# Kernel optimization log

Hardware: AMD Instinct MI355X
Metric: run time of the kernel (lower is better)

The kernel has to match this reference:

```python
import jax, jax.numpy as jnp
import numpy as np

KH, KW = 3, 3
STRIDE, PAD, DIL = 1, 1, 1


def setup_inputs() -> dict:
    key = jax.random.key(0)
    k1, k2, k3 = jax.random.split(key, 3)
    B, C, H, W, O = 8, 128, 64, 64, 128
    x = jax.random.normal(k1, (B, C, H, W), jnp.float32)
    # offset layout: [B, 2*K, Ho, Wo], pairs (dy, dx) per kernel tap
    offset = jax.random.normal(k2, (B, 2 * KH * KW, H, W), jnp.float32)
    n = C * KH * KW
    stdv = 1.0 / np.sqrt(n)
    weight = jax.random.uniform(k3, (O, C, KH, KW), jnp.float32, -stdv, stdv)
    bias = jnp.zeros((O,), jnp.float32)
    return {"x": x, "offset": offset, "weight": weight, "bias": bias}


def _deform_conv(x, offset, weight, bias):
    B, C, H, W = x.shape
    O = weight.shape[0]
    K = KH * KW
    Ho = (H + 2 * PAD - DIL * (KH - 1) - 1) // STRIDE + 1
    Wo = (W + 2 * PAD - DIL * (KW - 1) - 1) // STRIDE + 1

    off = offset.reshape(B, K, 2, Ho, Wo)  # (dy, dx) per tap

    # base sampling grid for each kernel tap: [K, Ho, Wo]
    hs = jnp.arange(Ho, dtype=jnp.float32) * STRIDE - PAD
    ws = jnp.arange(Wo, dtype=jnp.float32) * STRIDE - PAD
    ki = jnp.arange(KH, dtype=jnp.float32) * DIL
    kj = jnp.arange(KW, dtype=jnp.float32) * DIL
    base_y = (ki[:, None, None, None] + hs[None, None, :, None])  # [KH,1,Ho,1]
    base_x = (kj[None, :, None, None] + ws[None, None, None, :])  # [1,KW,1,Wo]
    base_y = jnp.broadcast_to(base_y, (KH, KW, Ho, Wo)).reshape(K, Ho, Wo)
    base_x = jnp.broadcast_to(base_x, (KH, KW, Ho, Wo)).reshape(K, Ho, Wo)

    py = base_y[None] + off[:, :, 0]  # [B,K,Ho,Wo]
    px = base_x[None] + off[:, :, 1]

    y0 = jnp.floor(py)
    x0 = jnp.floor(px)
    ly = py - y0  # fractional parts
    lx = px - x0
    y0i = y0.astype(jnp.int32)
    x0i = x0.astype(jnp.int32)

    flat = x.reshape(B, C, H * W)

    def gather(yi, xi, w):
        # zero outside the image (DCN zero-padding semantics)
        valid = (yi >= 0) & (yi < H) & (xi >= 0) & (xi < W)
        idx = jnp.clip(yi, 0, H - 1) * W + jnp.clip(xi, 0, W - 1)  # [B,K,Ho,Wo]
        g = jnp.take_along_axis(flat, idx.reshape(B, 1, -1), axis=2)
        g = g.reshape(B, C, K, Ho, Wo)
        wmask = (w * valid.astype(x.dtype))[:, None]  # [B,1,K,Ho,Wo]
        return g * wmask

    # bilinear accumulation over 4 corners -> im2col columns [B,C,K,Ho,Wo]
    cols = gather(y0i, x0i, (1 - ly) * (1 - lx))
    cols = cols + gather(y0i, x0i + 1, (1 - ly) * lx)
    cols = cols + gather(y0i + 1, x0i, ly * (1 - lx))
    cols = cols + gather(y0i + 1, x0i + 1, ly * lx)

    out = jnp.einsum('ock,bckhw->bohw', weight.reshape(O, C, K), cols)
    return out + bias[None, :, None, None]


def reference(x, offset, weight, bias):
    return _deform_conv(x, offset, weight, bias)
```

## Files before the change

kernel.cpp:

```cpp
#include <hip/hip_runtime.h>


#define BB 8
#define CC 128
#define HH 64
#define WW 64
#define OO 128
#define KTAPS 9

typedef __attribute__((ext_vector_type(8))) short bf16x8;
typedef __attribute__((ext_vector_type(4))) float f32x4;

__device__ __forceinline__ unsigned short f2bf(float f) {
    unsigned u = __float_as_uint(f);
    u += 0x7FFFu + ((u >> 16) & 1u);
    return (unsigned short)(u >> 16);
}
#if __has_builtin(__builtin_amdgcn_cvt_pk_bf16_f32)
typedef __attribute__((ext_vector_type(2))) __bf16 bf16x2_t;
__device__ __forceinline__ unsigned pack2bf(float lo, float hi) {
    bf16x2_t v = __builtin_amdgcn_cvt_pk_bf16_f32(lo, hi);
    unsigned r;
    __builtin_memcpy(&r, &v, 4);
    return r;
}
#else
__device__ __forceinline__ unsigned pack2bf(float lo, float hi) {
    return (unsigned)f2bf(lo) | ((unsigned)f2bf(hi) << 16);
}
#endif
__device__ __forceinline__ float bflo(unsigned p) { return __uint_as_float(p << 16); }
__device__ __forceinline__ float bfhi(unsigned p) { return __uint_as_float(p & 0xFFFF0000u); }

__global__ __launch_bounds__(256)
void prep_kernel(const float* __restrict__ x, const float* __restrict__ wgt,
                 unsigned short* __restrict__ xt, unsigned short* __restrict__ wpk) {
    const int t = threadIdx.x;
    if (blockIdx.x < 512) {
        __shared__ float tile[WW * 132];
        const int b = blockIdx.x >> 6;
        const int h = blockIdx.x & 63;
        const float* src = x + ((size_t)b * CC * HH + h) * WW;
        {
            const int wq = t & 15;
            const int cb = t >> 4;
#pragma unroll
            for (int it = 0; it < 8; ++it) {
                const int c = it * 16 + cb;
                const float4 v = *reinterpret_cast<const float4*>(src + (size_t)c * (HH * WW) + wq * 4);
                tile[(wq * 4 + 0) * 132 + c] = v.x;
                tile[(wq * 4 + 1) * 132 + c] = v.y;
                tile[(wq * 4 + 2) * 132 + c] = v.z;
                tile[(wq * 4 + 3) * 132 + c] = v.w;
            }
        }
        __syncthreads();
        unsigned short* dst = xt + ((size_t)b * HH + h) * WW * CC;
        {
            const int cg = t & 15;
            const int wb = t >> 4;
#pragma unroll
            for (int it = 0; it < 4; ++it) {
                const int w = it * 16 + wb;
                const float* tp = &tile[w * 132 + cg * 8];
                uint4 p;
                p.x = pack2bf(tp[0], tp[1]);
                p.y = pack2bf(tp[2], tp[3]);
                p.z = pack2bf(tp[4], tp[5]);
                p.w = pack2bf(tp[6], tp[7]);
                *reinterpret_cast<uint4*>(&dst[(size_t)w * CC + cg * 8]) = p;
            }
        }
    } else {
        const int id   = (blockIdx.x - 512) * 256 + t;
        const int lane = id & 63;
        const int frag = id >> 6;
        const int nt   = frag & 7;
        const int c0q  = (frag >> 3) & 3;
        const int tap  = frag >> 5;
        const int o    = (nt << 4) + (lane & 15);
        const int c    = (c0q << 5) + ((lane >> 4) << 3);
        const float* s = wgt + ((size_t)o * CC + c) * KTAPS + tap;
        unsigned u[4];
#pragma unroll
        for (int j = 0; j < 4; ++j)
            u[j] = pack2bf(s[(2 * j) * KTAPS], s[(2 * j + 1) * KTAPS]);
        *reinterpret_cast<uint4*>(wpk + (size_t)frag * 512 + lane * 8) =
            make_uint4(u[0], u[1], u[2], u[3]);
    }
}

__global__ __launch_bounds__(256, 2)
void dcn_mfma_kernel(const unsigned short* __restrict__ xt,
                     const unsigned short* __restrict__ wpk,
                     const float* __restrict__ offset,
                     const float* __restrict__ bias,
                     float* __restrict__ out) {
    __shared__ __align__(16) float smem_f[4 * 128 * 20];
    float2* sLL = reinterpret_cast<float2*>(smem_f);
    short2* sYX = reinterpret_cast<short2*>(smem_f + 1152);

    const int t  = threadIdx.x;
    const int b  = blockIdx.x >> 6;
    const int ho = blockIdx.x & 63;

    for (int s = t; s < KTAPS * 64; s += 256) {
        const int k  = s >> 6;
        const int wo = s & 63;
        const int ki = k / 3;
        const int kj = k - ki * 3;
        const float dy = offset[(((size_t)b * 18 + 2 * k    ) * 64 + ho) * 64 + wo];
        const float dx = offset[(((size_t)b * 18 + 2 * k + 1) * 64 + ho) * 64 + wo];
        const float py = (float)(ho - 1 + ki) + dy;
        const float px = (float)(wo - 1 + kj) + dx;
        const float y0f = floorf(py);
        const float x0f = floorf(px);
        sLL[s] = make_float2(py - y0f, px - x0f);
        sYX[s] = make_short2((short)(int)y0f, (short)(int)x0f);
    }
    __syncthreads();

    f32x4 acc[8];
#pragma unroll
    for (int nt = 0; nt < 8; ++nt) acc[nt] = (f32x4){0.f, 0.f, 0.f, 0.f};

    const int lane = t & 63;
    const int wave = t >> 6;
    const int lm   = lane & 15;
    const int quad = lane >> 4;
    const int q16  = quad * 16;
    const int lane16 = lane * 16;
    const char* xb = (const char*)(xt + (size_t)b * HH * WW * CC);
    const char* wb = (const char*)wpk;

    for (int tap = 0; tap < KTAPS; ++tap) {
        const int rec = (tap << 6) + (wave << 4) + lm;
        const float2 ll = sLL[rec];
        const short2 yx = sYX[rec];
        const int y0 = yx.x, x0 = yx.y;
        const int y1 = y0 + 1, x1 = x0 + 1;
        const float ly = ll.x, lx = ll.y;
        const bool vy0 = ((unsigned)y0 < (unsigned)HH);
        const bool vy1 = ((unsigned)y1 < (unsigned)HH);
        const bool vx0 = ((unsigned)x0 < (unsigned)WW);
        const bool vx1 = ((unsigned)x1 < (unsigned)WW);
        const float w00 = (vy0 && vx0) ? (1.f - ly) * (1.f - lx) : 0.f;
        const float w01 = (vy0 && vx1) ? (1.f - ly) * lx         : 0.f;
        const float w10 = (vy1 && vx0) ? ly * (1.f - lx)         : 0.f;
        const float w11 = (vy1 && vx1) ? ly * lx                 : 0.f;
        const int cy0 = min(max(y0, 0), HH - 1);
        const int cy1 = min(max(y1, 0), HH - 1);
        const int cx0 = min(max(x0, 0), WW - 1);
        const int cx1 = min(max(x1, 0), WW - 1);
        const char* base00 = xb + ((((cy0 << 6) + cx0) << 8) + q16);
        const char* base01 = xb + ((((cy0 << 6) + cx1) << 8) + q16);
        const char* base10 = xb + ((((cy1 << 6) + cx0) << 8) + q16);
        const char* base11 = xb + ((((cy1 << 6) + cx1) << 8) + q16);

        uint4 a00 = *reinterpret_cast<const uint4*>(base00);
        uint4 a01 = *reinterpret_cast<const uint4*>(base01);
        uint4 a10 = *reinterpret_cast<const uint4*>(base10);
        uint4 a11 = *reinterpret_cast<const uint4*>(base11);

#pragma unroll
        for (int c0q = 0; c0q < 4; ++c0q) {
            uint4 bfr[8];
            const char* wrow = wb + ((((tap << 5) + (c0q << 3))) << 10) + lane16;
#pragma unroll
            for (int nt = 0; nt < 8; ++nt)
                bfr[nt] = *reinterpret_cast<const uint4*>(wrow + (nt << 10));
            uint4 n00, n01, n10, n11;
            if (c0q < 3) {
                const int cb = (c0q + 1) << 6;
                n00 = *reinterpret_cast<const uint4*>(base00 + cb);
                n01 = *reinterpret_cast<const uint4*>(base01 + cb);
                n10 = *reinterpret_cast<const uint4*>(base10 + cb);
                n11 = *reinterpret_cast<const uint4*>(base11 + cb);
            }
            const unsigned* u00 = reinterpret_cast<const unsigned*>(&a00);
            const unsigned* u01 = reinterpret_cast<const unsigned*>(&a01);
            const unsigned* u10 = reinterpret_cast<const unsigned*>(&a10);
            const unsigned* u11 = reinterpret_cast<const unsigned*>(&a11);
            unsigned afu[4];
#pragma unroll
            for (int j = 0; j < 4; ++j) {
                const float rl = w00 * bflo(u00[j]) + w01 * bflo(u01[j])
                               + w10 * bflo(u10[j]) + w11 * bflo(u11[j]);
                const float rh = w00 * bfhi(u00[j]) + w01 * bfhi(u01[j])
                               + w10 * bfhi(u10[j]) + w11 * bfhi(u11[j]);
                afu[j] = pack2bf(rl, rh);
            }
            bf16x8 afrag;
            __builtin_memcpy(&afrag, afu, 16);
#pragma unroll
            for (int nt = 0; nt < 8; ++nt) {
                bf16x8 bfrag;
                __builtin_memcpy(&bfrag, &bfr[nt], 16);
                acc[nt] = __builtin_amdgcn_mfma_f32_16x16x32_bf16(afrag, bfrag, acc[nt], 0, 0, 0);
            }
            if (c0q < 3) { a00 = n00; a01 = n01; a10 = n10; a11 = n11; }
        }
    }

    __syncthreads();
    float* scr = smem_f + wave * (128 * 20);
#pragma unroll
    for (int nt = 0; nt < 8; ++nt) {
        const int o_l = (nt << 4) + lm;
        *reinterpret_cast<float4*>(&scr[o_l * 20 + (quad << 2)]) =
            make_float4(acc[nt][0], acc[nt][1], acc[nt][2], acc[nt][3]);
    }
#pragma unroll
    for (int h = 0; h < 2; ++h) {
        const int o = (h << 6) + lane;
        const float bv = bias[o];
        float* op = out + (((size_t)(b * OO + o) * HH + ho) << 6) + (wave << 4);
        const float* sr = scr + o * 20;
#pragma unroll
        for (int j = 0; j < 4; ++j) {
            const float4 f = *reinterpret_cast<const float4*>(sr + j * 4);
            *reinterpret_cast<float4*>(op + j * 4) =
                make_float4(f.x + bv, f.y + bv, f.z + bv, f.w + bv);
        }
    }
}

extern "C" void kernel_launch(void* const* d_in, const int* in_sizes, int n_in,
                              void* d_out, int out_size, void* d_ws, size_t ws_size,
                              hipStream_t stream) {
    const float* x      = (const float*)d_in[0];
    const float* offset = (const float*)d_in[1];
    const float* wgt    = (const float*)d_in[2];
    const float* bias   = (const float*)d_in[3];
    float* out = (float*)d_out;

    unsigned short* xt  = (unsigned short*)d_ws;
    unsigned short* wpk = xt + (size_t)BB * HH * WW * CC;

    hipLaunchKernelGGL(prep_kernel, dim3(512 + 72), dim3(256), 0, stream, x, wgt, xt, wpk);
    hipLaunchKernelGGL(dcn_mfma_kernel, dim3(BB * HH), dim3(256), 0, stream,
                       xt, wpk, offset, bias, out);
}
```

Before: 132.4 us.

## Split output channels across two blocks, prefetch next tap, remap block order

The grid doubles so that each block computes half of the output channels (64 instead of 128). This halves the accumulators and weight-fragment registers and raises the launch-bounds occupancy target to 4 blocks. The gather for the next tap's first channel chunk is now issued during the last chunk of the current tap, hiding load latency across tap boundaries. Block indices are swizzled so that blocks sharing the same image row are spread across the grid. The cost is that every bilinear sample and its interpolation is computed twice, once per channel half.

Result: slower. 158.2 us (+19.5%).

```diff
diff --git a/kernel.cpp b/kernel.cpp
--- a/kernel.cpp
+++ b/kernel.cpp
@@ -90,19 +90,52 @@
     }
 }
 
-__global__ __launch_bounds__(256, 2)
+__device__ __forceinline__ void decode_tap(const float2* __restrict__ sLL,
+                                           const short2* __restrict__ sYX,
+                                           int rec, int q16,
+                                           unsigned& o00, unsigned& o01,
+                                           unsigned& o10, unsigned& o11,
+                                           float& w00, float& w01,
+                                           float& w10, float& w11) {
+    const float2 ll = sLL[rec];
+    const short2 yx = sYX[rec];
+    const int y0 = yx.x, x0 = yx.y;
+    const int y1 = y0 + 1, x1 = x0 + 1;
+    const float ly = ll.x, lx = ll.y;
+    const bool vy0 = ((unsigned)y0 < (unsigned)HH);
+    const bool vy1 = ((unsigned)y1 < (unsigned)HH);
+    const bool vx0 = ((unsigned)x0 < (unsigned)WW);
+    const bool vx1 = ((unsigned)x1 < (unsigned)WW);
+    w00 = (vy0 && vx0) ? (1.f - ly) * (1.f - lx) : 0.f;
+    w01 = (vy0 && vx1) ? (1.f - ly) * lx         : 0.f;
+    w10 = (vy1 && vx0) ? ly * (1.f - lx)         : 0.f;
+    w11 = (vy1 && vx1) ? ly * lx                 : 0.f;
+    const int cy0 = min(max(y0, 0), HH - 1);
+    const int cy1 = min(max(y1, 0), HH - 1);
+    const int cx0 = min(max(x0, 0), WW - 1);
+    const int cx1 = min(max(x1, 0), WW - 1);
+    o00 = (unsigned)(((((cy0 << 6) + cx0)) << 8) + q16);
+    o01 = (unsigned)(((((cy0 << 6) + cx1)) << 8) + q16);
+    o10 = (unsigned)(((((cy1 << 6) + cx0)) << 8) + q16);
+    o11 = (unsigned)(((((cy1 << 6) + cx1)) << 8) + q16);
+}
+
+__global__ __launch_bounds__(256, 4)
 void dcn_mfma_kernel(const unsigned short* __restrict__ xt,
                      const unsigned short* __restrict__ wpk,
                      const float* __restrict__ offset,
                      const float* __restrict__ bias,
                      float* __restrict__ out) {
-    __shared__ __align__(16) float smem_f[4 * 128 * 20];
+    __shared__ __align__(16) float smem_f[4 * 64 * 20];
     float2* sLL = reinterpret_cast<float2*>(smem_f);
     short2* sYX = reinterpret_cast<short2*>(smem_f + 1152);
 
-    const int t  = threadIdx.x;
-    const int b  = blockIdx.x >> 6;
-    const int ho = blockIdx.x & 63;
+    const int t    = threadIdx.x;
+    const int bid0 = blockIdx.x;
+    const int nid  = ((bid0 & 7) << 7) | (bid0 >> 3);
+    const int oh   = nid >> 9;
+    const int b    = (nid >> 6) & 7;
+    const int ho   = nid & 63;
 
     for (int s = t; s < KTAPS * 64; s += 256) {
         const int k  = s >> 6;
@@ -120,9 +153,9 @@
     }
     __syncthreads();
 
-    f32x4 acc[8];
-#pragma unroll
-    for (int nt = 0; nt < 8; ++nt) acc[nt] = (f32x4){0.f, 0.f, 0.f, 0.f};
+    f32x4 acc[4];
+#pragma unroll
+    for (int nt = 0; nt < 4; ++nt) acc[nt] = (f32x4){0.f, 0.f, 0.f, 0.f};
 
     const int lane = t & 63;
     const int wave = t >> 6;
@@ -133,50 +166,42 @@
     const char* xb = (const char*)(xt + (size_t)b * HH * WW * CC);
     const char* wb = (const char*)wpk;
 
+    unsigned o00, o01, o10, o11;
+    float w00, w01, w10, w11;
+    decode_tap(sLL, sYX, (wave << 4) + lm, q16, o00, o01, o10, o11, w00, w01, w10, w11);
+    uint4 a00 = *reinterpret_cast<const uint4*>(xb + o00);
+    uint4 a01 = *reinterpret_cast<const uint4*>(xb + o01);
+    uint4 a10 = *reinterpret_cast<const uint4*>(xb + o10);
+    uint4 a11 = *reinterpret_cast<const uint4*>(xb + o11);
+
     for (int tap = 0; tap < KTAPS; ++tap) {
-        const int rec = (tap << 6) + (wave << 4) + lm;
-        const float2 ll = sLL[rec];
-        const short2 yx = sYX[rec];
-        const int y0 = yx.x, x0 = yx.y;
-        const int y1 = y0 + 1, x1 = x0 + 1;
-        const float ly = ll.x, lx = ll.y;
-        const bool vy0 = ((unsigned)y0 < (unsigned)HH);
-        const bool vy1 = ((unsigned)y1 < (unsigned)HH);
-        const bool vx0 = ((unsigned)x0 < (unsigned)WW);
-        const bool vx1 = ((unsigned)x1 < (unsigned)WW);
-        const float w00 = (vy0 && vx0) ? (1.f - ly) * (1.f - lx) : 0.f;
-        const float w01 = (vy0 && vx1) ? (1.f - ly) * lx         : 0.f;
-        const float w10 = (vy1 && vx0) ? ly * (1.f - lx)         : 0.f;
-        const float w11 = (vy1 && vx1) ? ly * lx                 : 0.f;
-        const int cy0 = min(max(y0, 0), HH - 1);
-        const int cy1 = min(max(y1, 0), HH - 1);
-        const int cx0 = min(max(x0, 0), WW - 1);
-        const int cx1 = min(max(x1, 0), WW - 1);
-        const char* base00 = xb + ((((cy0 << 6) + cx0) << 8) + q16);
-        const char* base01 = xb + ((((cy0 << 6) + cx1) << 8) + q16);
-        const char* base10 = xb + ((((cy1 << 6) + cx0) << 8) + q16);
-        const char* base11 = xb + ((((cy1 << 6) + cx1) << 8) + q16);
-
-        uint4 a00 = *reinterpret_cast<const uint4*>(base00);
-        uint4 a01 = *reinterpret_cast<const uint4*>(base01);
-        uint4 a10 = *reinterpret_cast<const uint4*>(base10);
-        uint4 a11 = *reinterpret_cast<const uint4*>(base11);
-
 #pragma unroll
         for (int c0q = 0; c0q < 4; ++c0q) {
-            uint4 bfr[8];
-            const char* wrow = wb + ((((tap << 5) + (c0q << 3))) << 10) + lane16;
-#pragma unroll
-            for (int nt = 0; nt < 8; ++nt)
+            uint4 bfr[4];
+            const int fragbase = (((tap << 2) + c0q) << 3) + (oh << 2);
+            const char* wrow = wb + ((size_t)fragbase << 10) + lane16;
+#pragma unroll
+            for (int nt = 0; nt < 4; ++nt)
                 bfr[nt] = *reinterpret_cast<const uint4*>(wrow + (nt << 10));
+
             uint4 n00, n01, n10, n11;
+            unsigned no00 = 0, no01 = 0, no10 = 0, no11 = 0;
+            float nw00 = 0.f, nw01 = 0.f, nw10 = 0.f, nw11 = 0.f;
             if (c0q < 3) {
                 const int cb = (c0q + 1) << 6;
-                n00 = *reinterpret_cast<const uint4*>(base00 + cb);
-                n01 = *reinterpret_cast<const uint4*>(base01 + cb);
-                n10 = *reinterpret_cast<const uint4*>(base10 + cb);
-                n11 = *reinterpret_cast<const uint4*>(base11 + cb);
-            }
+                n00 = *reinterpret_cast<const uint4*>(xb + o00 + cb);
+                n01 = *reinterpret_cast<const uint4*>(xb + o01 + cb);
+                n10 = *reinterpret_cast<const uint4*>(xb + o10 + cb);
+                n11 = *reinterpret_cast<const uint4*>(xb + o11 + cb);
+            } else if (tap < KTAPS - 1) {
+                decode_tap(sLL, sYX, ((tap + 1) << 6) + (wave << 4) + lm, q16,
+                           no00, no01, no10, no11, nw00, nw01, nw10, nw11);
+                n00 = *reinterpret_cast<const uint4*>(xb + no00);
+                n01 = *reinterpret_cast<const uint4*>(xb + no01);
+                n10 = *reinterpret_cast<const uint4*>(xb + no10);
+                n11 = *reinterpret_cast<const uint4*>(xb + no11);
+            }
+
             const unsigned* u00 = reinterpret_cast<const unsigned*>(&a00);
             const unsigned* u01 = reinterpret_cast<const unsigned*>(&a01);
             const unsigned* u10 = reinterpret_cast<const unsigned*>(&a10);
@@ -193,29 +218,35 @@
             bf16x8 afrag;
             __builtin_memcpy(&afrag, afu, 16);
 #pragma unroll
-            for (int nt = 0; nt < 8; ++nt) {
+            for (int nt = 0; nt < 4; ++nt) {
                 bf16x8 bfrag;
                 __builtin_memcpy(&bfrag, &bfr[nt], 16);
                 acc[nt] = __builtin_amdgcn_mfma_f32_16x16x32_bf16(afrag, bfrag, acc[nt], 0, 0, 0);
             }
-            if (c0q < 3) { a00 = n00; a01 = n01; a10 = n10; a11 = n11; }
+
+            if (c0q < 3) {
+                a00 = n00; a01 = n01; a10 = n10; a11 = n11;
+            } else if (tap < KTAPS - 1) {
+                a00 = n00; a01 = n01; a10 = n10; a11 = n11;
+                o00 = no00; o01 = no01; o10 = no10; o11 = no11;
+                w00 = nw00; w01 = nw01; w10 = nw10; w11 = nw11;
+            }
         }
     }
 
     __syncthreads();
-    float* scr = smem_f + wave * (128 * 20);
-#pragma unroll
-    for (int nt = 0; nt < 8; ++nt) {
+    float* scr = smem_f + wave * (64 * 20);
+#pragma unroll
+    for (int nt = 0; nt < 4; ++nt) {
         const int o_l = (nt << 4) + lm;
         *reinterpret_cast<float4*>(&scr[o_l * 20 + (quad << 2)]) =
             make_float4(acc[nt][0], acc[nt][1], acc[nt][2], acc[nt][3]);
     }
-#pragma unroll
-    for (int h = 0; h < 2; ++h) {
-        const int o = (h << 6) + lane;
+    {
+        const int o = (oh << 6) + lane;
         const float bv = bias[o];
         float* op = out + (((size_t)(b * OO + o) * HH + ho) << 6) + (wave << 4);
-        const float* sr = scr + o * 20;
+        const float* sr = scr + lane * 20;
 #pragma unroll
         for (int j = 0; j < 4; ++j) {
             const float4 f = *reinterpret_cast<const float4*>(sr + j * 4);
@@ -238,6 +269,6 @@
     unsigned short* wpk = xt + (size_t)BB * HH * WW * CC;
 
     hipLaunchKernelGGL(prep_kernel, dim3(512 + 72), dim3(256), 0, stream, x, wgt, xt, wpk);
-    hipLaunchKernelGGL(dcn_mfma_kernel, dim3(BB * HH), dim3(256), 0, stream,
+    hipLaunchKernelGGL(dcn_mfma_kernel, dim3(2 * BB * HH), dim3(256), 0, stream,
                        xt, wpk, offset, bias, out);
 }
```
